# Optimization experiments

Measured on AMD Instinct MI355X. Metric: run time of the kernel, lower is better.

Reference implementation:

```python
import jax, jax.numpy as jnp
import numpy as np
import math

N, C, W, H = 8, 1024, 1024, 16
D = C // H  # head size = 64


def setup_inputs() -> dict:
    key = jax.random.key(0)
    ks = jax.random.split(key, 7)
    s = 1.0 / math.sqrt(C)
    return {
        "hidden_states": jax.random.normal(ks[0], (N, C, W), jnp.float32),
        "attention_mask": jnp.zeros((N, 1, 1, W), jnp.float32),
        "wq": jax.random.normal(ks[1], (C, C), jnp.float32) * s,
        "bq": jax.random.normal(ks[2], (C,), jnp.float32) * 0.02,
        "wk": jax.random.normal(ks[3], (C, C), jnp.float32) * s,
        "bk": jax.random.normal(ks[4], (C,), jnp.float32) * 0.02,
        "wv": jax.random.normal(ks[5], (C, C), jnp.float32) * s,
        "bv": jax.random.normal(ks[6], (C,), jnp.float32) * 0.02,
    }


def reference(hidden_states, attention_mask, wq, bq, wk, bk, wv, bv):
    # conv1d(kernel=1, groups=1) == per-position GEMM: [N,C,W] x [Cout,Cin] -> [N,Cout,W]
    q = jnp.einsum('ncw,oc->now', hidden_states, wq) + bq[None, :, None]
    k = jnp.einsum('ncw,oc->now', hidden_states, wk) + bk[None, :, None]
    v = jnp.einsum('ncw,oc->now', hidden_states, wv) + bv[None, :, None]
    # split heads: [N,C,W] -> [N,H,D,W]
    q = q.reshape(N, H, D, W).transpose(0, 1, 3, 2)  # [N,H,W,D]
    k = k.reshape(N, H, D, W)                         # [N,H,D,W]
    v = v.reshape(N, H, D, W).transpose(0, 1, 3, 2)  # [N,H,W,D]
    scores = jnp.einsum('nhqd,nhdk->nhqk', q, k) / math.sqrt(D)
    scores = scores + attention_mask  # broadcast [N,1,1,W]
    probs = jax.nn.softmax(scores, axis=-1)
    ctx = jnp.einsum('nhqk,nhkd->nhqd', probs, v)    # [N,H,W,D]
    # merge heads back to [N,C,W]
    return ctx.transpose(0, 1, 3, 2).reshape(N, C, W)
```

## Files before the change

kernel.cpp:

```cpp
#include <hip/hip_runtime.h>
#include <hip/hip_bf16.h>

typedef __bf16 bf16x8 __attribute__((ext_vector_type(8)));
typedef __bf16 bf16x4 __attribute__((ext_vector_type(4)));
typedef float f32x4 __attribute__((ext_vector_type(4)));

#define N_ 8
#define C_ 1024
#define W_ 1024
#define H_ 16
#define D_ 64

typedef __attribute__((address_space(3))) void lds_void;
typedef const __attribute__((address_space(1))) void gbl_void;
static __device__ __forceinline__ void gload_lds16(const void* g, void* l) {
    __builtin_amdgcn_global_load_lds((gbl_void*)g, (lds_void*)l, 16, 0, 0);
}

__global__ __launch_bounds__(256)
void convert_w(const float* __restrict__ s0, const float* __restrict__ s1,
               const float* __restrict__ s2, __bf16* __restrict__ dst) {
    const float* s = blockIdx.y == 0 ? s0 : (blockIdx.y == 1 ? s1 : s2);
    __bf16* d = dst + (long)blockIdx.y * C_ * C_;
    const long i = ((long)blockIdx.x * 256 + threadIdx.x) * 8;
    f32x4 a = *(const f32x4*)(const void*)(s + i);
    f32x4 b = *(const f32x4*)(const void*)(s + i + 4);
    bf16x8 v;
    #pragma unroll
    for (int t = 0; t < 4; ++t) { v[t] = (__bf16)a[t]; v[t + 4] = (__bf16)b[t]; }
    *(bf16x8*)(void*)(d + i) = v;
}

__global__ __launch_bounds__(256)
void transpose_x(const float* __restrict__ in, __bf16* __restrict__ outp) {
    __shared__ float tile[64][68];
    const long bin  = (long)blockIdx.z * C_ * W_;
    const long bout = (long)blockIdx.z * W_ * C_;
    const int w0 = blockIdx.x * 64, c0 = blockIdx.y * 64;
    const int t = threadIdx.x;
    const int rr = t >> 4;
    const int cg = (t & 15) * 4;
    #pragma unroll
    for (int it = 0; it < 4; ++it) {
        const int cr = it * 16 + rr;
        f32x4 v = *(const f32x4*)(const void*)(in + bin + (long)(c0 + cr) * W_ + w0 + cg);
        *(f32x4*)&tile[cr][cg] = v;
    }
    __syncthreads();
    #pragma unroll
    for (int it = 0; it < 4; ++it) {
        const int wr = it * 16 + rr;
        bf16x4 o;
        #pragma unroll
        for (int u = 0; u < 4; ++u) o[u] = (__bf16)tile[cg + u][wr];
        *(bf16x4*)(void*)(outp + bout + (long)(w0 + wr) * C_ + c0 + cg) = o;
    }
}

template<int OUT_T>
static __device__ __forceinline__
void gemm_body(const __bf16* __restrict__ Aw, const __bf16* __restrict__ Xn,
               const float* __restrict__ bias, __bf16* __restrict__ Pn,
               const int o0, const int w0,
               __bf16* __restrict__ As, __bf16* __restrict__ Bs) {
    constexpr int BK = 64;
    const int tid = threadIdx.x;
    const int wv = tid >> 6, lane = tid & 63;
    const int l15 = lane & 15, quad = lane >> 4;
    const int wr = (wv >> 1) * 64, wc = (wv & 1) * 64;
    const int lr8 = lane >> 3;
    const int lp = lane & 7;

    f32x4 acc[4][4] = {};

    for (int k0 = 0; k0 < C_; k0 += BK) {
        #pragma unroll
        for (int j = 0; j < 4; ++j) {
            const int seg = wv * 4 + j;
            const int r = seg * 8 + lr8;
            const int q = lp ^ (r & 7);
            gload_lds16(Aw + (long)(o0 + r) * C_ + k0 + q * 8, As + seg * 512);
            gload_lds16(Xn + (long)(w0 + r) * C_ + k0 + q * 8, Bs + seg * 512);
        }
        __syncthreads();
        bf16x8 af[4][2], bf[4][2];
        #pragma unroll
        for (int mt = 0; mt < 4; ++mt) {
            const int R = wr + mt * 16 + l15;
            #pragma unroll
            for (int s = 0; s < 2; ++s) {
                const int pos = (s * 4 + quad) ^ (R & 7);
                af[mt][s] = *(const bf16x8*)(const void*)&As[R * 64 + pos * 8];
            }
        }
        #pragma unroll
        for (int nt = 0; nt < 4; ++nt) {
            const int R = wc + nt * 16 + l15;
            #pragma unroll
            for (int s = 0; s < 2; ++s) {
                const int pos = (s * 4 + quad) ^ (R & 7);
                bf[nt][s] = *(const bf16x8*)(const void*)&Bs[R * 64 + pos * 8];
            }
        }
        #pragma unroll
        for (int s = 0; s < 2; ++s)
            #pragma unroll
            for (int mt = 0; mt < 4; ++mt)
                #pragma unroll
                for (int nt = 0; nt < 4; ++nt) {
                    if (OUT_T == 0)
                        acc[mt][nt] = __builtin_amdgcn_mfma_f32_16x16x32_bf16(af[mt][s], bf[nt][s], acc[mt][nt], 0, 0, 0);
                    else
                        acc[mt][nt] = __builtin_amdgcn_mfma_f32_16x16x32_bf16(bf[nt][s], af[mt][s], acc[mt][nt], 0, 0, 0);
                }
        __syncthreads();
    }

    #pragma unroll
    for (int mt = 0; mt < 4; ++mt) {
        #pragma unroll
        for (int nt = 0; nt < 4; ++nt) {
            #pragma unroll
            for (int rg = 0; rg < 4; ++rg) {
                if (OUT_T == 0) {
                    const int col = w0 + wc + nt * 16 + l15;
                    const int row = o0 + wr + mt * 16 + quad * 4 + rg;
                    Pn[(long)row * W_ + col] = (__bf16)(acc[mt][nt][rg] + bias[row]);
                } else {
                    const int o = o0 + wr + mt * 16 + l15;
                    const int w = w0 + wc + nt * 16 + quad * 4 + rg;
                    Pn[(long)w * C_ + o] = (__bf16)(acc[mt][nt][rg] + bias[o]);
                }
            }
        }
    }
}

__global__ __launch_bounds__(256)
void gemm_qkv(const __bf16* __restrict__ Wb, const __bf16* __restrict__ Xt,
              const float* __restrict__ bq, const float* __restrict__ bk,
              const float* __restrict__ bv,
              __bf16* __restrict__ Qt, __bf16* __restrict__ Kt,
              __bf16* __restrict__ Vb) {
    __shared__ __align__(16) __bf16 As[128 * 64];
    __shared__ __align__(16) __bf16 Bs[128 * 64];
    const int f = blockIdx.x;
    const int n = f & 7;
    const int j = f >> 3;
    const int which = j >> 6;
    const int t = j & 63;
    const int o0 = (t >> 3) * 128;
    const int w0 = (t & 7) * 128;
    const size_t SZ = (size_t)C_ * W_;
    const size_t WSZ = (size_t)C_ * C_;
    const __bf16* Xn = Xt + (size_t)n * SZ;
    const __bf16* Aw = Wb + (size_t)which * WSZ;
    if (which < 2)
        gemm_body<1>(Aw, Xn, which ? bk : bq, (which ? Kt : Qt) + n * SZ, o0, w0, As, Bs);
    else
        gemm_body<0>(Aw, Xn, bv, Vb + n * SZ, o0, w0, As, Bs);
}

__global__ __launch_bounds__(256)
void flash_attn(const __bf16* __restrict__ Qt,
                const __bf16* __restrict__ Kt,
                const __bf16* __restrict__ V,
                const float* __restrict__ mask,
                float* __restrict__ out) {
    constexpr int PSTR = 72;
    __shared__ __align__(16) __bf16 Pl[4][32][PSTR];
    __shared__ __align__(16) __bf16 Ks[2][64 * 64];
    __shared__ __align__(16) __bf16 Vs[2][64 * 64];

    const int f = blockIdx.x;
    const int g = (f & 7) + ((f >> 6) << 3);
    const int m = (f >> 3) & 7;
    const int n = g >> 4, h = g & 15;
    const int q0 = m * 128;

    const int tid = threadIdx.x;
    const int wave = tid >> 6, lane = tid & 63;
    const int l15 = lane & 15, quad = lane >> 4;
    const int lr8 = lane >> 3, lp = lane & 7;
    const long nqk = (long)n * W_ * C_;
    const long nv = (long)n * C_ * W_;
    const int hD = h * D_;
    const float* mrow = mask + (long)n * W_;
    constexpr float SC = 0.125f * 1.44269504f;

    bf16x8 aq[2][2];
    #pragma unroll
    for (int qs = 0; qs < 2; ++qs)
        #pragma unroll
        for (int dc = 0; dc < 2; ++dc)
            aq[qs][dc] = *(const bf16x8*)(const void*)
                (Qt + nqk + (long)(q0 + wave * 32 + qs * 16 + l15) * C_ + hD + dc * 32 + quad * 8);

    f32x4 o_acc[2][4] = {};
    float l_ln[2][4] = {};

    auto stage = [&](int kt, int b) {
        #pragma unroll
        for (int jj = 0; jj < 2; ++jj) {
            const int seg = wave * 2 + jj;
            const int r = seg * 8 + lr8;
            const int q = lp ^ (r & 7);
            gload_lds16(Kt + nqk + (long)(kt + r) * C_ + hD + q * 8, &Ks[b][seg * 512]);
            gload_lds16(V + nv + (long)(hD + r) * W_ + kt + q * 8, &Vs[b][seg * 512]);
        }
    };

    stage(0, 0);

    for (int ti = 0; ti < W_ / 64; ++ti) {
        const int kt = ti * 64;
        const int cur = ti & 1;
        asm volatile("s_waitcnt vmcnt(0)" ::: "memory");
        __syncthreads();
        if (ti + 1 < W_ / 64) stage(kt + 64, cur ^ 1);

        bf16x8 bk[4][2], bv[4][2];
        #pragma unroll
        for (int ks = 0; ks < 4; ++ks)
            #pragma unroll
            for (int dc = 0; dc < 2; ++dc) {
                const int R = ks * 16 + l15;
                const int pos = (dc * 4 + quad) ^ (R & 7);
                bk[ks][dc] = *(const bf16x8*)(const void*)&Ks[cur][R * 64 + pos * 8];
            }
        #pragma unroll
        for (int ds = 0; ds < 4; ++ds)
            #pragma unroll
            for (int kc = 0; kc < 2; ++kc) {
                const int R = ds * 16 + l15;
                const int pos = (kc * 4 + quad) ^ (R & 7);
                bv[ds][kc] = *(const bf16x8*)(const void*)&Vs[cur][R * 64 + pos * 8];
            }
        float mk2[4];
        #pragma unroll
        for (int ks = 0; ks < 4; ++ks) mk2[ks] = mrow[kt + ks * 16 + l15] * 1.44269504f;

        #pragma unroll
        for (int qs = 0; qs < 2; ++qs) {
            f32x4 s[4] = {};
            #pragma unroll
            for (int ks = 0; ks < 4; ++ks)
                #pragma unroll
                for (int dc = 0; dc < 2; ++dc)
                    s[ks] = __builtin_amdgcn_mfma_f32_16x16x32_bf16(aq[qs][dc], bk[ks][dc], s[ks], 0, 0, 0);
            #pragma unroll
            for (int ks = 0; ks < 4; ++ks)
                #pragma unroll
                for (int rg = 0; rg < 4; ++rg)
                    s[ks][rg] = __builtin_exp2f(s[ks][rg] * SC + mk2[ks]);
            #pragma unroll
            for (int rg = 0; rg < 4; ++rg)
                l_ln[qs][rg] += (s[0][rg] + s[1][rg]) + (s[2][rg] + s[3][rg]);
            #pragma unroll
            for (int ks = 0; ks < 4; ++ks)
                #pragma unroll
                for (int rg = 0; rg < 4; ++rg)
                    Pl[wave][qs * 16 + quad * 4 + rg][ks * 16 + l15] = (__bf16)s[ks][rg];
            bf16x8 ap[2];
            #pragma unroll
            for (int kc = 0; kc < 2; ++kc)
                ap[kc] = *(const bf16x8*)(const void*)&Pl[wave][qs * 16 + l15][kc * 32 + quad * 8];
            #pragma unroll
            for (int ds = 0; ds < 4; ++ds)
                #pragma unroll
                for (int kc = 0; kc < 2; ++kc)
                    o_acc[qs][ds] = __builtin_amdgcn_mfma_f32_16x16x32_bf16(ap[kc], bv[ds][kc], o_acc[qs][ds], 0, 0, 0);
        }
    }

    #pragma unroll
    for (int qs = 0; qs < 2; ++qs) {
        float inv[4];
        #pragma unroll
        for (int rg = 0; rg < 4; ++rg) {
            float l = l_ln[qs][rg];
            #pragma unroll
            for (int off = 1; off < 16; off <<= 1)
                l += __shfl_xor(l, off, 64);
            inv[rg] = 1.0f / l;
        }
        #pragma unroll
        for (int ds = 0; ds < 4; ++ds)
            #pragma unroll
            for (int rg = 0; rg < 4; ++rg)
                out[nv + (long)(hD + ds * 16 + l15) * W_ + q0 + wave * 32 + qs * 16 + quad * 4 + rg]
                    = o_acc[qs][ds][rg] * inv[rg];
    }
}

extern "C" void kernel_launch(void* const* d_in, const int* in_sizes, int n_in,
                              void* d_out, int out_size, void* d_ws, size_t ws_size,
                              hipStream_t stream) {
    (void)in_sizes; (void)n_in; (void)out_size; (void)ws_size;
    const float* hs   = (const float*)d_in[0];
    const float* mask = (const float*)d_in[1];
    const float* wq   = (const float*)d_in[2];
    const float* bq   = (const float*)d_in[3];
    const float* wk   = (const float*)d_in[4];
    const float* bk   = (const float*)d_in[5];
    const float* wv   = (const float*)d_in[6];
    const float* bv   = (const float*)d_in[7];
    float* out = (float*)d_out;

    const size_t SZ = (size_t)N_ * C_ * W_;
    const size_t WSZ = (size_t)C_ * C_;
    __bf16* Wb = (__bf16*)d_ws;
    __bf16* Xt = Wb + 3 * WSZ;
    __bf16* Qt = Xt + SZ;
    __bf16* Kt = Qt + SZ;
    __bf16* Vb = Kt + SZ;

    convert_w<<<dim3(512, 3), 256, 0, stream>>>(wq, wk, wv, Wb);
    transpose_x<<<dim3(W_ / 64, C_ / 64, N_), 256, 0, stream>>>(hs, Xt);

    gemm_qkv<<<dim3(1536), 256, 0, stream>>>(Wb, Xt, bq, bk, bv, Qt, Kt, Vb);

    flash_attn<<<dim3(1024), 256, 0, stream>>>(Qt, Kt, Vb, mask, out);
}
```

Measured before the change: 251.7 us.

## Transpose score MFMA so P is written as packed rows into swizzled LDS

Swaps the operands of the QK^T MFMA so each lane holds four consecutive key scores for a single query row. This lets the probabilities be written to LDS as packed bf16x4 stores into an XOR-swizzled, unpadded buffer instead of scalar transposed stores. It also loads the mask as float4 vectors. The row-sum is now accumulated per lane and reduced with two shuffles, plus one shuffle per output element. The point is to cut LDS store instructions, bank conflicts and shuffle work in the softmax-to-PV handoff, at the cost of more intricate indexing.

```diff
diff --git a/kernel.cpp b/kernel.cpp
--- a/kernel.cpp
+++ b/kernel.cpp
@@ -167,8 +167,7 @@
                 const __bf16* __restrict__ V,
                 const float* __restrict__ mask,
                 float* __restrict__ out) {
-    constexpr int PSTR = 72;
-    __shared__ __align__(16) __bf16 Pl[4][32][PSTR];
+    __shared__ __align__(16) __bf16 Pl[4 * 16 * 64];
     __shared__ __align__(16) __bf16 Ks[2][64 * 64];
     __shared__ __align__(16) __bf16 Vs[2][64 * 64];
 
@@ -187,6 +186,11 @@
     const int hD = h * D_;
     const float* mrow = mask + (long)n * W_;
     constexpr float SC = 0.125f * 1.44269504f;
+    constexpr float L2E = 1.44269504f;
+
+    char* plb = (char*)Pl + wave * 2048;
+    const int swz = (l15 & 7) << 4;
+    const long plrow = l15 * 128;
 
     bf16x8 aq[2][2];
     #pragma unroll
@@ -197,7 +201,7 @@
                 (Qt + nqk + (long)(q0 + wave * 32 + qs * 16 + l15) * C_ + hD + dc * 32 + quad * 8);
 
     f32x4 o_acc[2][4] = {};
-    float l_ln[2][4] = {};
+    float l_ln[2] = {};
 
     auto stage = [&](int kt, int b) {
         #pragma unroll
@@ -236,9 +240,10 @@
                 const int pos = (kc * 4 + quad) ^ (R & 7);
                 bv[ds][kc] = *(const bf16x8*)(const void*)&Vs[cur][R * 64 + pos * 8];
             }
-        float mk2[4];
-        #pragma unroll
-        for (int ks = 0; ks < 4; ++ks) mk2[ks] = mrow[kt + ks * 16 + l15] * 1.44269504f;
+        f32x4 mk[4];
+        #pragma unroll
+        for (int ks = 0; ks < 4; ++ks)
+            mk[ks] = *(const f32x4*)(const void*)(mrow + kt + ks * 16 + quad * 4);
 
         #pragma unroll
         for (int qs = 0; qs < 2; ++qs) {
@@ -247,24 +252,25 @@
             for (int ks = 0; ks < 4; ++ks)
                 #pragma unroll
                 for (int dc = 0; dc < 2; ++dc)
-                    s[ks] = __builtin_amdgcn_mfma_f32_16x16x32_bf16(aq[qs][dc], bk[ks][dc], s[ks], 0, 0, 0);
-            #pragma unroll
-            for (int ks = 0; ks < 4; ++ks)
+                    s[ks] = __builtin_amdgcn_mfma_f32_16x16x32_bf16(bk[ks][dc], aq[qs][dc], s[ks], 0, 0, 0);
+            #pragma unroll
+            for (int ks = 0; ks < 4; ++ks) {
                 #pragma unroll
                 for (int rg = 0; rg < 4; ++rg)
-                    s[ks][rg] = __builtin_exp2f(s[ks][rg] * SC + mk2[ks]);
-            #pragma unroll
-            for (int rg = 0; rg < 4; ++rg)
-                l_ln[qs][rg] += (s[0][rg] + s[1][rg]) + (s[2][rg] + s[3][rg]);
-            #pragma unroll
-            for (int ks = 0; ks < 4; ++ks)
-                #pragma unroll
-                for (int rg = 0; rg < 4; ++rg)
-                    Pl[wave][qs * 16 + quad * 4 + rg][ks * 16 + l15] = (__bf16)s[ks][rg];
+                    s[ks][rg] = __builtin_exp2f(s[ks][rg] * SC + mk[ks][rg] * L2E);
+                l_ln[qs] += (s[ks][0] + s[ks][1]) + (s[ks][2] + s[ks][3]);
+            }
+            #pragma unroll
+            for (int ks = 0; ks < 4; ++ks) {
+                bf16x4 p4;
+                #pragma unroll
+                for (int rg = 0; rg < 4; ++rg) p4[rg] = (__bf16)s[ks][rg];
+                *(bf16x4*)(void*)(plb + plrow + (((ks * 32 + quad * 8) ^ swz))) = p4;
+            }
             bf16x8 ap[2];
             #pragma unroll
             for (int kc = 0; kc < 2; ++kc)
-                ap[kc] = *(const bf16x8*)(const void*)&Pl[wave][qs * 16 + l15][kc * 32 + quad * 8];
+                ap[kc] = *(const bf16x8*)(const void*)(plb + plrow + (((kc * 64 + quad * 16) ^ swz)));
             #pragma unroll
             for (int ds = 0; ds < 4; ++ds)
                 #pragma unroll
@@ -275,21 +281,18 @@
 
     #pragma unroll
     for (int qs = 0; qs < 2; ++qs) {
-        float inv[4];
+        float l = l_ln[qs];
+        l += __shfl_xor(l, 16, 64);
+        l += __shfl_xor(l, 32, 64);
+        const float linv = 1.0f / l;
         #pragma unroll
         for (int rg = 0; rg < 4; ++rg) {
-            float l = l_ln[qs][rg];
-            #pragma unroll
-            for (int off = 1; off < 16; off <<= 1)
-                l += __shfl_xor(l, off, 64);
-            inv[rg] = 1.0f / l;
-        }
-        #pragma unroll
-        for (int ds = 0; ds < 4; ++ds)
-            #pragma unroll
-            for (int rg = 0; rg < 4; ++rg)
+            const float inv = __shfl(linv, quad * 4 + rg, 64);
+            #pragma unroll
+            for (int ds = 0; ds < 4; ++ds)
                 out[nv + (long)(hD + ds * 16 + l15) * W_ + q0 + wave * 32 + qs * 16 + quad * 4 + rg]
-                    = o_acc[qs][ds][rg] * inv[rg];
+                    = o_acc[qs][ds][rg] * inv;
+        }
     }
 }
 
```

Result: no change. 248.7 us (-1.2%).
